# Optimization experiments

Hardware: AMD Instinct MI355X
Metric: run time of the kernel (lower is better)

The kernel has to match this reference:

```python
import jax, jax.numpy as jnp
import numpy as np

WS = 8      # window_size
NH = 8      # n_heads
EPS = 1e-06


def _rel_coords(ws):
    # Swin-style relative position index table, matches torch buffer construction
    c = np.stack(np.meshgrid(np.arange(ws), np.arange(ws), indexing='ij'))  # [2,ws,ws]
    c = c.reshape(2, -1)                      # [2, L]
    rel = c[:, :, None] - c[:, None, :]       # [2, L, L]
    rel = rel.transpose(1, 2, 0) + (ws - 1)   # [L, L, 2]
    rel[:, :, 0] *= 2 * ws - 1
    return jnp.asarray(rel.sum(-1), dtype=jnp.int32)  # [L, L]


def rms_film(x, t, gw, bw):
    # x: [B,C,H,W], t: [B,d_t]; RMS over channel dim, FiLM scale/shift from t
    g = (t @ gw.T)[:, :, None, None]
    b = (t @ bw.T)[:, :, None, None]
    return g * x * jax.lax.rsqrt(jnp.mean(x * x, axis=1, keepdims=True) + EPS) + b


def window_attn(x, wq, wk, wv, wo_w, wo_b, rpb):
    B, C, H, W = x.shape
    h, w = H // WS, W // WS
    L = WS * WS
    dh = C // NH
    # partition into windows: [B, h, w, L, C]
    xw = x.reshape(B, C, h, WS, w, WS).transpose(0, 2, 4, 3, 5, 1).reshape(B, h, w, L, C)

    def heads(p):
        y = xw @ p.T  # Linear, no bias
        return y.reshape(B, h, w, L, NH, dh).transpose(0, 1, 2, 4, 3, 5)  # [B,h,w,n,L,dh]

    q, k, v = heads(wq), heads(wk), heads(wv)
    bias = rpb[:, _rel_coords(WS)]  # [NH, L, L] gather from bias table
    attn = jnp.einsum('bhwnld,bhwnmd->bhwnlm', q, k) / float(np.sqrt(dh)) + bias
    o = jnp.einsum('bhwnlm,bhwnmd->bhwnld', jax.nn.softmax(attn, axis=-1), v)
    # merge windows, channel order (n c): [B, NH*dh, H, W]
    o = o.reshape(B, h, w, NH, WS, WS, dh).transpose(0, 3, 6, 1, 4, 2, 5).reshape(B, C, H, W)
    # 1x1 conv output projection (with bias)
    return jnp.einsum('bchw,oc->bohw', o, wo_w) + wo_b[None, :, None, None]


def convnext(x, t, dw_w, dw_b, gw, bw, w1, b1, w2, b2):
    # 7x7 depthwise conv, pad 3
    y = jax.lax.conv_general_dilated(
        x, dw_w, window_strides=(1, 1), padding=[(3, 3), (3, 3)],
        dimension_numbers=('NCHW', 'OIHW', 'NCHW'), feature_group_count=x.shape[1])
    y = y + dw_b[None, :, None, None]
    y = rms_film(y, t, gw, bw).transpose(0, 2, 3, 1)  # -> NHWC
    y = jax.nn.gelu(y @ w1.T + b1, approximate=False) @ w2.T + b2
    return y.transpose(0, 3, 1, 2)


def setup_inputs() -> dict:
    key = jax.random.key(0)
    ks = jax.random.split(key, 16)
    D, DT, B, H, W = 256, 256, 8, 128, 128
    DH = 4 * D
    n = lambda k, s: jax.random.normal(k, s, jnp.float32) * 0.02
    return dict(
        x=jax.random.normal(ks[0], (B, D, H, W), jnp.float32),
        t=jax.random.normal(ks[1], (B, DT), jnp.float32),
        an_g=n(ks[2], (D, DT)), an_b=n(ks[3], (D, DT)),
        wq=n(ks[4], (D, D)), wk=n(ks[5], (D, D)), wv=n(ks[6], (D, D)),
        wo_w=n(ks[7], (D, D)), wo_b=jnp.zeros((D,), jnp.float32),
        rpb=n(ks[8], (NH, (2 * WS - 1) ** 2)),
        dw_w=n(ks[9], (D, 1, 7, 7)), dw_b=jnp.zeros((D,), jnp.float32),
        fn_g=n(ks[10], (D, DT)), fn_b=n(ks[11], (D, DT)),
        w1=n(ks[12], (DH, D)), b1=jnp.zeros((DH,), jnp.float32),
        w2=n(ks[13], (D, DH)), b2=jnp.zeros((D,), jnp.float32))


def reference(x, t, an_g, an_b, wq, wk, wv, wo_w, wo_b, rpb,
              dw_w, dw_b, fn_g, fn_b, w1, b1, w2, b2):
    x = x + window_attn(rms_film(x, t, an_g, an_b), wq, wk, wv, wo_w, wo_b, rpb)
    return x + convnext(x, t, dw_w, dw_b, fn_g, fn_b, w1, b1, w2, b2)
```

## Files before the change

### kernel.cpp

```cpp
#include <hip/hip_runtime.h>
#include <math.h>

typedef __attribute__((ext_vector_type(8))) short bf16x8_t;
typedef __attribute__((ext_vector_type(4))) float f32x4;

__device__ __forceinline__ unsigned short f2bf(float f) {
  unsigned int u = __builtin_bit_cast(unsigned int, f);
  u += 0x7FFFu + ((u >> 16) & 1u);
  return (unsigned short)(u >> 16);
}
__device__ __forceinline__ float bf2f(unsigned short h) {
  unsigned int u = ((unsigned int)h) << 16;
  return __builtin_bit_cast(float, u);
}

typedef const __attribute__((address_space(1))) void* as1cv;
typedef __attribute__((address_space(3))) void* as3v;

__device__ __forceinline__ void gld_lds16(const unsigned short* g, unsigned short* l) {
  __builtin_amdgcn_global_load_lds((as1cv)g, (as3v)l, 16, 0, 0);
}

__global__ __launch_bounds__(256) void tvec_kernel(const float* __restrict__ t,
    const float* __restrict__ an_g, const float* __restrict__ an_b,
    const float* __restrict__ fn_g, const float* __restrict__ fn_b,
    float* __restrict__ gvec) {
  int d = threadIdx.x;
  int b = blockIdx.x;
  int m = blockIdx.y;
  __shared__ float ts[256];
  ts[d] = t[b * 256 + d];
  __syncthreads();
  const float* W = (m == 0) ? an_g : (m == 1) ? an_b : (m == 2) ? fn_g : fn_b;
  float acc = 0.f;
  #pragma unroll 8
  for (int k = 0; k < 256; ++k) acc += ts[k] * W[d * 256 + k];
  gvec[(m * 8 + b) * 256 + d] = acc;
}

__global__ __launch_bounds__(256) void wconv_kernel(const float* __restrict__ wq,
    const float* __restrict__ wk, const float* __restrict__ wv, const float* __restrict__ wo,
    const float* __restrict__ w1, const float* __restrict__ w2,
    unsigned short* __restrict__ outp) {
  int i = blockIdx.x * 256 + threadIdx.x;
  const float* src; int off;
  if      (i <  65536) { src = wq; off = 0; }
  else if (i < 131072) { src = wk; off = 65536; }
  else if (i < 196608) { src = wv; off = 131072; }
  else if (i < 262144) { src = wo; off = 196608; }
  else if (i < 524288) { src = w1; off = 262144; }
  else                 { src = w2; off = 524288; }
  outp[i] = f2bf(src[i - off]);
}

template<int IS_BF, int WX>
__global__ __launch_bounds__(256) void film_kernel(const void* __restrict__ in_,
    const float* __restrict__ gvec, int gsel, unsigned short* __restrict__ outbf,
    unsigned short* __restrict__ xbf) {
  const float* inf = (const float*)in_;
  const unsigned short* inb = (const unsigned short*)in_;
  int blk = blockIdx.x;
  int b = blk >> 8;
  int p0 = (blk & 255) << 6;
  int lane = threadIdx.x & 63;
  int cg = threadIdx.x >> 6;
  __shared__ unsigned short vals[64][264];
  __shared__ float ssred[4][64];
  __shared__ float rinvs[64];
  size_t base = ((size_t)b << 22) + p0;
  float ss = 0.f;
  #pragma unroll 4
  for (int ci = 0; ci < 64; ++ci) {
    int c = (cg << 6) + ci;
    size_t idx = base + ((size_t)c << 14) + lane;
    float v = IS_BF ? bf2f(inb[idx]) : inf[idx];
    ss += v * v;
    unsigned short hv = f2bf(v);
    vals[lane][c] = hv;
    if (WX) xbf[idx] = hv;
  }
  ssred[cg][lane] = ss;
  __syncthreads();
  if (threadIdx.x < 64) {
    float s = ssred[0][threadIdx.x] + ssred[1][threadIdx.x] + ssred[2][threadIdx.x] + ssred[3][threadIdx.x];
    rinvs[threadIdx.x] = rsqrtf(s * (1.0f / 256.0f) + 1e-6f);
  }
  __syncthreads();
  int pix = threadIdx.x >> 2;
  int c0 = (threadIdx.x & 3) << 6;
  float rv = rinvs[pix];
  const float* gp = gvec + ((gsel * 2 + 0) * 8 + b) * 256;
  const float* bp = gvec + ((gsel * 2 + 1) * 8 + b) * 256;
  unsigned short* orow = outbf + (((size_t)b << 14) + p0 + pix) * 256 + c0;
  #pragma unroll
  for (int ch = 0; ch < 8; ++ch) {
    bf16x8_t pack;
    #pragma unroll
    for (int e = 0; e < 8; ++e) {
      int c = c0 + ch * 8 + e;
      float v = bf2f(vals[pix][c]);
      float o = gp[c] * v * rv + bp[c];
      pack[e] = (short)f2bf(o);
    }
    *(bf16x8_t*)(orow + ch * 8) = pack;
  }
}

template<int DO_GELU>
__global__ __launch_bounds__(256) void gemm_kernel(const unsigned short* __restrict__ A,
    const unsigned short* __restrict__ Bw, const float* __restrict__ bias,
    unsigned short* __restrict__ outp, int K, int N) {
  __shared__ unsigned short As[128 * 64];
  __shared__ unsigned short Bs[128 * 64];
  int tid = threadIdx.x;
  int m0 = blockIdx.x << 7;
  int n0 = blockIdx.y << 7;
  int w = tid >> 6, lane = tid & 63;
  int wm = (w >> 1) << 6, wn = (w & 1) << 6;
  f32x4 acc[4][4];
  #pragma unroll
  for (int mi = 0; mi < 4; ++mi)
    #pragma unroll
    for (int ni = 0; ni < 4; ++ni)
      acc[mi][ni] = (f32x4){0.f, 0.f, 0.f, 0.f};

  for (int k0 = 0; k0 < K; k0 += 64) {
    #pragma unroll
    for (int r2 = 0; r2 < 4; ++r2) {
      int linear = (r2 << 8) + tid;
      int row = linear >> 3;
      int ch = linear & 7;
      gld_lds16(A  + (size_t)(m0 + row) * K + k0 + ch * 8, As + linear * 8);
      gld_lds16(Bw + (size_t)(n0 + row) * K + k0 + ch * 8, Bs + linear * 8);
    }
    __syncthreads();
    #pragma unroll
    for (int kk = 0; kk < 64; kk += 32) {
      bf16x8_t af[4], bq[4];
      int lr = lane & 15;
      int lk = ((lane >> 4) << 3) + kk;
      #pragma unroll
      for (int mi = 0; mi < 4; ++mi)
        af[mi] = *(const bf16x8_t*)(As + ((wm + (mi << 4) + lr) << 6) + lk);
      #pragma unroll
      for (int ni = 0; ni < 4; ++ni)
        bq[ni] = *(const bf16x8_t*)(Bs + ((wn + (ni << 4) + lr) << 6) + lk);
      #pragma unroll
      for (int mi = 0; mi < 4; ++mi)
        #pragma unroll
        for (int ni = 0; ni < 4; ++ni)
          acc[mi][ni] = __builtin_amdgcn_mfma_f32_16x16x32_bf16(af[mi], bq[ni], acc[mi][ni], 0, 0, 0);
    }
    __syncthreads();
  }
  int lr = lane & 15, lg = lane >> 4;
  #pragma unroll
  for (int mi = 0; mi < 4; ++mi) {
    #pragma unroll
    for (int ni = 0; ni < 4; ++ni) {
      int col = n0 + wn + (ni << 4) + lr;
      int row = m0 + wm + (mi << 4) + (lg << 2);
      f32x4 a = acc[mi][ni];
      #pragma unroll
      for (int i = 0; i < 4; ++i) {
        float v = a[i];
        if (DO_GELU) {
          v += bias[col];
          v = 0.5f * v * (1.0f + erff(v * 0.70710678118654752f));
        }
        outp[(size_t)(row + i) * N + col] = f2bf(v);
      }
    }
  }
}

__global__ __launch_bounds__(256) void gemm_qkv_kernel(const unsigned short* __restrict__ A,
    const unsigned short* __restrict__ Bw, unsigned short* __restrict__ outq,
    unsigned short* __restrict__ outk, unsigned short* __restrict__ outvt) {
  __shared__ unsigned short smem[16384];
  unsigned short* As = smem;
  unsigned short* Bs = smem + 8192;
  const int K = 256;
  int tid = threadIdx.x;
  int m0 = blockIdx.x << 7;
  int n0 = blockIdx.y << 7;
  int w = tid >> 6, lane = tid & 63;
  int wm = (w >> 1) << 6, wn = (w & 1) << 6;
  f32x4 acc[4][4];
  #pragma unroll
  for (int mi = 0; mi < 4; ++mi)
    #pragma unroll
    for (int ni = 0; ni < 4; ++ni)
      acc[mi][ni] = (f32x4){0.f, 0.f, 0.f, 0.f};

  for (int k0 = 0; k0 < K; k0 += 64) {
    #pragma unroll
    for (int r2 = 0; r2 < 4; ++r2) {
      int linear = (r2 << 8) + tid;
      int row = linear >> 3;
      int ch = linear & 7;
      gld_lds16(A  + (size_t)(m0 + row) * K + k0 + ch * 8, As + linear * 8);
      gld_lds16(Bw + (size_t)(n0 + row) * K + k0 + ch * 8, Bs + linear * 8);
    }
    __syncthreads();
    #pragma unroll
    for (int kk = 0; kk < 64; kk += 32) {
      bf16x8_t af[4], bq[4];
      int lr = lane & 15;
      int lk = ((lane >> 4) << 3) + kk;
      #pragma unroll
      for (int mi = 0; mi < 4; ++mi)
        af[mi] = *(const bf16x8_t*)(As + ((wm + (mi << 4) + lr) << 6) + lk);
      #pragma unroll
      for (int ni = 0; ni < 4; ++ni)
        bq[ni] = *(const bf16x8_t*)(Bs + ((wn + (ni << 4) + lr) << 6) + lk);
      #pragma unroll
      for (int mi = 0; mi < 4; ++mi)
        #pragma unroll
        for (int ni = 0; ni < 4; ++ni)
          acc[mi][ni] = __builtin_amdgcn_mfma_f32_16x16x32_bf16(af[mi], bq[ni], acc[mi][ni], 0, 0, 0);
    }
    __syncthreads();
  }

  int lr = lane & 15, lg = lane >> 4;
  if (n0 < 512) {
    unsigned short* dst = (n0 < 256) ? outq : outk;
    #pragma unroll
    for (int mi = 0; mi < 4; ++mi) {
      #pragma unroll
      for (int ni = 0; ni < 4; ++ni) {
        int col = (n0 & 255) + wn + (ni << 4) + lr;
        int row = m0 + wm + (mi << 4) + (lg << 2);
        f32x4 a = acc[mi][ni];
        #pragma unroll
        for (int i = 0; i < 4; ++i)
          dst[(size_t)(row + i) * 256 + col] = f2bf(a[i]);
      }
    }
  } else {
    #pragma unroll
    for (int mi = 0; mi < 4; ++mi)
      #pragma unroll
      for (int ni = 0; ni < 4; ++ni) {
        int cl = wn + (ni << 4) + lr;
        int rl = wm + (mi << 4) + (lg << 2);
        f32x4 a = acc[mi][ni];
        #pragma unroll
        for (int i = 0; i < 4; ++i)
          smem[cl * 128 + rl + i] = f2bf(a[i]);
      }
    __syncthreads();
    int cl = tid >> 1;
    int half = tid & 1;
    int b = m0 >> 14;
    int pix = (m0 & 16383) + half * 64;
    int c = (n0 - 512) + cl;
    const unsigned short* srow = smem + cl * 128 + half * 64;
    unsigned short* orow = outvt + ((size_t)b * 256 + c) * 16384 + pix;
    #pragma unroll
    for (int jj = 0; jj < 8; ++jj)
      *(bf16x8_t*)(orow + jj * 8) = *(const bf16x8_t*)(srow + jj * 8);
  }
}

__global__ __launch_bounds__(256) void gemm_wof_kernel(const unsigned short* __restrict__ A,
    const unsigned short* __restrict__ Bw, const float* __restrict__ bias,
    const unsigned short* __restrict__ xbf, unsigned short* __restrict__ outp) {
  __shared__ unsigned short smem[16384];
  unsigned short* As = smem;
  unsigned short* Bs = smem + 8192;
  const int K = 256;
  int tid = threadIdx.x;
  int m0 = blockIdx.x << 7;
  int n0 = blockIdx.y << 7;
  int w = tid >> 6, lane = tid & 63;
  int wm = (w >> 1) << 6, wn = (w & 1) << 6;
  f32x4 acc[4][4];
  #pragma unroll
  for (int mi = 0; mi < 4; ++mi)
    #pragma unroll
    for (int ni = 0; ni < 4; ++ni)
      acc[mi][ni] = (f32x4){0.f, 0.f, 0.f, 0.f};

  for (int k0 = 0; k0 < K; k0 += 64) {
    #pragma unroll
    for (int r2 = 0; r2 < 4; ++r2) {
      int linear = (r2 << 8) + tid;
      int row = linear >> 3;
      int ch = linear & 7;
      gld_lds16(A  + (size_t)(m0 + row) * K + k0 + ch * 8, As + linear * 8);
      gld_lds16(Bw + (size_t)(n0 + row) * K + k0 + ch * 8, Bs + linear * 8);
    }
    __syncthreads();
    #pragma unroll
    for (int kk = 0; kk < 64; kk += 32) {
      bf16x8_t af[4], bq[4];
      int lr = lane & 15;
      int lk = ((lane >> 4) << 3) + kk;
      #pragma unroll
      for (int mi = 0; mi < 4; ++mi)
        af[mi] = *(const bf16x8_t*)(As + ((wm + (mi << 4) + lr) << 6) + lk);
      #pragma unroll
      for (int ni = 0; ni < 4; ++ni)
        bq[ni] = *(const bf16x8_t*)(Bs + ((wn + (ni << 4) + lr) << 6) + lk);
      #pragma unroll
      for (int mi = 0; mi < 4; ++mi)
        #pragma unroll
        for (int ni = 0; ni < 4; ++ni)
          acc[mi][ni] = __builtin_amdgcn_mfma_f32_16x16x32_bf16(af[mi], bq[ni], acc[mi][ni], 0, 0, 0);
    }
    __syncthreads();
  }

  int lr = lane & 15, lg = lane >> 4;
  #pragma unroll
  for (int mi = 0; mi < 4; ++mi)
    #pragma unroll
    for (int ni = 0; ni < 4; ++ni) {
      int cl = wn + (ni << 4) + lr;
      int rl = wm + (mi << 4) + (lg << 2);
      f32x4 a = acc[mi][ni];
      #pragma unroll
      for (int i = 0; i < 4; ++i)
        smem[cl * 128 + rl + i] = f2bf(a[i]);
    }
  __syncthreads();

  int cl = tid >> 1;
  int half = tid & 1;
  int b = m0 >> 14;
  int pix = (m0 & 16383) + half * 64;
  int c = n0 + cl;
  const unsigned short* srow = smem + cl * 128 + half * 64;
  size_t gbase = ((size_t)b * 256 + c) * 16384 + pix;
  const unsigned short* xrow = xbf + gbase;
  unsigned short* orow = outp + gbase;
  float bb = bias[c];
  #pragma unroll
  for (int jj = 0; jj < 8; ++jj) {
    bf16x8_t sv = *(const bf16x8_t*)(srow + jj * 8);
    bf16x8_t xv = *(const bf16x8_t*)(xrow + jj * 8);
    bf16x8_t ov;
    #pragma unroll
    for (int e = 0; e < 8; ++e)
      ov[e] = (short)f2bf(bf2f((unsigned short)sv[e]) + bf2f((unsigned short)xv[e]) + bb);
    *(bf16x8_t*)(orow + jj * 8) = ov;
  }
}

__global__ __launch_bounds__(256) void gemm2f_kernel(const unsigned short* __restrict__ A,
    const unsigned short* __restrict__ Bw, const float* __restrict__ bias,
    const unsigned short* __restrict__ x1, float* __restrict__ outp, int m_base) {
  __shared__ unsigned short smem[16384];
  unsigned short* As = smem;
  unsigned short* Bs = smem + 8192;
  const int K = 1024, N = 256;
  int tid = threadIdx.x;
  int m0 = blockIdx.x << 7;
  int n0 = blockIdx.y << 7;
  int w = tid >> 6, lane = tid & 63;
  int wm = (w >> 1) << 6, wn = (w & 1) << 6;
  f32x4 acc[4][4];
  #pragma unroll
  for (int mi = 0; mi < 4; ++mi)
    #pragma unroll
    for (int ni = 0; ni < 4; ++ni)
      acc[mi][ni] = (f32x4){0.f, 0.f, 0.f, 0.f};

  for (int k0 = 0; k0 < K; k0 += 64) {
    #pragma unroll
    for (int r2 = 0; r2 < 4; ++r2) {
      int linear = (r2 << 8) + tid;
      int row = linear >> 3;
      int ch = linear & 7;
      gld_lds16(A  + (size_t)(m0 + row) * K + k0 + ch * 8, As + linear * 8);
      gld_lds16(Bw + (size_t)(n0 + row) * K + k0 + ch * 8, Bs + linear * 8);
    }
    __syncthreads();
    #pragma unroll
    for (int kk = 0; kk < 64; kk += 32) {
      bf16x8_t af[4], bq[4];
      int lr = lane & 15;
      int lk = ((lane >> 4) << 3) + kk;
      #pragma unroll
      for (int mi = 0; mi < 4; ++mi)
        af[mi] = *(const bf16x8_t*)(As + ((wm + (mi << 4) + lr) << 6) + lk);
      #pragma unroll
      for (int ni = 0; ni < 4; ++ni)
        bq[ni] = *(const bf16x8_t*)(Bs + ((wn + (ni << 4) + lr) << 6) + lk);
      #pragma unroll
      for (int mi = 0; mi < 4; ++mi)
        #pragma unroll
        for (int ni = 0; ni < 4; ++ni)
          acc[mi][ni] = __builtin_amdgcn_mfma_f32_16x16x32_bf16(af[mi], bq[ni], acc[mi][ni], 0, 0, 0);
    }
    __syncthreads();
  }

  int lr = lane & 15, lg = lane >> 4;
  #pragma unroll
  for (int mi = 0; mi < 4; ++mi)
    #pragma unroll
    for (int ni = 0; ni < 4; ++ni) {
      int cl = wn + (ni << 4) + lr;
      int rl = wm + (mi << 4) + (lg << 2);
      f32x4 a = acc[mi][ni];
      #pragma unroll
      for (int i = 0; i < 4; ++i)
        smem[cl * 128 + rl + i] = f2bf(a[i]);
    }
  __syncthreads();

  int cl = tid >> 1;
  int half = tid & 1;
  int pglob0 = m_base + m0;
  int b = pglob0 >> 14;
  int pix = (pglob0 & 16383) + half * 64;
  int c = n0 + cl;
  const unsigned short* srow = smem + cl * 128 + half * 64;
  size_t gbase = ((size_t)b * 256 + c) * 16384 + pix;
  const unsigned short* xrow = x1 + gbase;
  float* orow = outp + gbase;
  float bb = bias[c];
  #pragma unroll
  for (int jj = 0; jj < 8; ++jj) {
    bf16x8_t sv = *(const bf16x8_t*)(srow + jj * 8);
    bf16x8_t xv = *(const bf16x8_t*)(xrow + jj * 8);
    #pragma unroll
    for (int e = 0; e < 8; ++e)
      orow[jj * 8 + e] = bf2f((unsigned short)sv[e]) + bf2f((unsigned short)xv[e]) + bb;
  }
}

__global__ __launch_bounds__(256, 4) void attn_kernel(const unsigned short* __restrict__ qg,
    const unsigned short* __restrict__ kg, const unsigned short* __restrict__ vt,
    const float* __restrict__ rpb, unsigned short* __restrict__ og) {
  __shared__ float rpbf[1800];
  __shared__ unsigned short pbuf[4][16 * 72];
  int wi = (blockIdx.x & 7) * 256 + (blockIdx.x >> 3);
  int b = wi >> 8, wh = (wi >> 4) & 15, ww = wi & 15;
  int tid = threadIdx.x;
  int w = tid >> 6, lane = tid & 63;
  int g = lane >> 4, lr = lane & 15;
  for (int idx = tid; idx < 1800; idx += 256) rpbf[idx] = rpb[idx];
  __syncthreads();

  int rowpix = (wh * 8) * 128 + ww * 8;
  size_t ibase = ((size_t)b << 14) + rowpix;
  unsigned short* pb = pbuf[w];
  const float scale = 0.17677669529663689f;

  #pragma unroll 1
  for (int hh = 0; hh < 2; ++hh) {
    int h = w * 2 + hh;
    bf16x8_t qf[4], kf[4];
    #pragma unroll
    for (int t = 0; t < 4; ++t) {
      size_t tok = ibase + (size_t)(t * 2 + (lr >> 3)) * 128 + (lr & 7);
      qf[t] = *(const bf16x8_t*)(qg + tok * 256 + h * 32 + g * 8);
      kf[t] = *(const bf16x8_t*)(kg + tok * 256 + h * 32 + g * 8);
    }
    bf16x8_t vfr[2][2];
    #pragma unroll
    for (int ks = 0; ks < 2; ++ks)
      #pragma unroll
      for (int dt = 0; dt < 2; ++dt) {
        size_t plane = (size_t)b * 256 + h * 32 + dt * 16 + lr;
        vfr[ks][dt] = *(const bf16x8_t*)(vt + (plane << 14) + rowpix + (size_t)(ks * 4 + g) * 128);
      }
    const float* rb = &rpbf[h * 225];

    #pragma unroll 1
    for (int qt = 0; qt < 4; ++qt) {
      f32x4 sacc[4];
      #pragma unroll
      for (int kt = 0; kt < 4; ++kt)
        sacc[kt] = __builtin_amdgcn_mfma_f32_16x16x32_bf16(qf[qt], kf[kt],
                     (f32x4){0.f, 0.f, 0.f, 0.f}, 0, 0, 0);
      float sums[4];
      #pragma unroll
      for (int i = 0; i < 4; ++i) {
        int q = qt * 16 + g * 4 + i;
        int il = q >> 3, jl = q & 7;
        float v[4];
        #pragma unroll
        for (int kt = 0; kt < 4; ++kt) {
          int kv = kt * 16 + lr;
          v[kt] = sacc[kt][i] * scale + rb[(il - (kv >> 3) + 7) * 15 + (jl - (kv & 7) + 7)];
        }
        float mx = fmaxf(fmaxf(v[0], v[1]), fmaxf(v[2], v[3]));
        mx = fmaxf(mx, __shfl_xor(mx, 1));
        mx = fmaxf(mx, __shfl_xor(mx, 2));
        mx = fmaxf(mx, __shfl_xor(mx, 4));
        mx = fmaxf(mx, __shfl_xor(mx, 8));
        float sm = 0.f;
        #pragma unroll
        for (int kt = 0; kt < 4; ++kt) { v[kt] = __expf(v[kt] - mx); sm += v[kt]; }
        sm += __shfl_xor(sm, 1);
        sm += __shfl_xor(sm, 2);
        sm += __shfl_xor(sm, 4);
        sm += __shfl_xor(sm, 8);
        sums[i] = sm;
        #pragma unroll
        for (int kt = 0; kt < 4; ++kt)
          pb[(g * 4 + i) * 72 + kt * 16 + lr] = f2bf(v[kt]);
      }
      f32x4 oacc[2] = {(f32x4){0.f, 0.f, 0.f, 0.f}, (f32x4){0.f, 0.f, 0.f, 0.f}};
      #pragma unroll
      for (int ks = 0; ks < 2; ++ks) {
        bf16x8_t pf = *(const bf16x8_t*)(pb + lr * 72 + ks * 32 + g * 8);
        oacc[0] = __builtin_amdgcn_mfma_f32_16x16x32_bf16(pf, vfr[ks][0], oacc[0], 0, 0, 0);
        oacc[1] = __builtin_amdgcn_mfma_f32_16x16x32_bf16(pf, vfr[ks][1], oacc[1], 0, 0, 0);
      }
      #pragma unroll
      for (int i = 0; i < 4; ++i) {
        int q = qt * 16 + g * 4 + i;
        float inv = 1.0f / sums[i];
        size_t tok = ibase + (size_t)(q >> 3) * 128 + (q & 7);
        unsigned int packed0 = f2bf(oacc[0][i] * inv);
        unsigned int packed1 = f2bf(oacc[1][i] * inv);
        og[tok * 256 + h * 32 + lr] = (unsigned short)packed0;
        og[tok * 256 + h * 32 + 16 + lr] = (unsigned short)packed1;
      }
    }
  }
}

__global__ __launch_bounds__(256) void dwconv_kernel(const unsigned short* __restrict__ x1,
    const float* __restrict__ w, const float* __restrict__ bias, unsigned short* __restrict__ outp) {
  int bc = blockIdx.y;
  int c = bc & 255;
  int y0 = blockIdx.x << 6;
  __shared__ unsigned short tile[70 * 144];
  __shared__ float wf[49];
  const unsigned short* plane = x1 + ((size_t)bc << 14);
  int tid = threadIdx.x;

  for (int idx = tid; idx < 70 * 16; idx += 256) {
    int row = idx >> 4, ch = idx & 15;
    int gy = y0 - 3 + row;
    bf16x8_t v = (bf16x8_t){0, 0, 0, 0, 0, 0, 0, 0};
    if (gy >= 0 && gy < 128) v = *(const bf16x8_t*)(plane + gy * 128 + ch * 8);
    *(bf16x8_t*)(&tile[row * 144 + 8 + ch * 8]) = v;
  }
  for (int idx = tid; idx < 70 * 6; idx += 256) {
    int row = idx / 6, e = idx % 6;
    int col = (e < 3) ? (5 + e) : (133 + e);
    tile[row * 144 + col] = 0;
  }
  if (tid < 49) wf[tid] = w[c * 49 + tid];
  __syncthreads();

  int r = tid >> 2;
  int c0 = (tid & 3) << 5;
  float acc[32];
  float bb = bias[c];
  #pragma unroll
  for (int i = 0; i < 32; ++i) acc[i] = bb;

  #pragma unroll
  for (int u = 0; u < 7; ++u) {
    const unsigned short* rowp = &tile[(r + u) * 144 + c0];
    float f[48];
    #pragma unroll
    for (int k = 0; k < 6; ++k) {
      bf16x8_t v = *(const bf16x8_t*)(rowp + k * 8);
      #pragma unroll
      for (int e = 0; e < 8; ++e) f[k * 8 + e] = bf2f((unsigned short)v[e]);
    }
    #pragma unroll
    for (int t = 0; t < 7; ++t) {
      float wv = wf[u * 7 + t];
      #pragma unroll
      for (int i = 0; i < 32; ++i) acc[i] += f[i + 5 + t] * wv;
    }
  }

  unsigned short* orow = outp + ((size_t)bc << 14) + (size_t)(y0 + r) * 128 + c0;
  #pragma unroll
  for (int k = 0; k < 4; ++k) {
    bf16x8_t v;
    #pragma unroll
    for (int e = 0; e < 8; ++e) v[e] = (short)f2bf(acc[k * 8 + e]);
    *(bf16x8_t*)(orow + k * 8) = v;
  }
}

extern "C" void kernel_launch(void* const* d_in, const int* in_sizes, int n_in,
                              void* d_out, int out_size, void* d_ws, size_t ws_size,
                              hipStream_t stream) {
  const float* x    = (const float*)d_in[0];
  const float* t    = (const float*)d_in[1];
  const float* an_g = (const float*)d_in[2];
  const float* an_b = (const float*)d_in[3];
  const float* wq   = (const float*)d_in[4];
  const float* wk   = (const float*)d_in[5];
  const float* wv   = (const float*)d_in[6];
  const float* wo_w = (const float*)d_in[7];
  const float* wo_b = (const float*)d_in[8];
  const float* rpb  = (const float*)d_in[9];
  const float* dw_w = (const float*)d_in[10];
  const float* dw_b = (const float*)d_in[11];
  const float* fn_g = (const float*)d_in[12];
  const float* fn_b = (const float*)d_in[13];
  const float* w1   = (const float*)d_in[14];
  const float* b1   = (const float*)d_in[15];
  const float* w2   = (const float*)d_in[16];
  const float* b2   = (const float*)d_in[17];
  float* outp = (float*)d_out;

  char* ws = (char*)d_ws;
  const size_t MB = 1024ull * 1024ull;
  float* gvec = (float*)ws;
  unsigned short* wbf = (unsigned short*)(ws + 32768);
  unsigned short* P = (unsigned short*)(ws + 2 * MB);
  unsigned short* Q = (unsigned short*)(ws + 66 * MB);
  unsigned short* R = (unsigned short*)(ws + 130 * MB);
  unsigned short* xbf  = (unsigned short*)d_out;
  unsigned short* vbuf = (unsigned short*)((char*)d_out + 64 * MB);

  unsigned short* wo_bf = wbf + 196608;
  unsigned short* w1_bf = wbf + 262144;
  unsigned short* w2_bf = wbf + 524288;

  tvec_kernel<<<dim3(8, 4), 256, 0, stream>>>(t, an_g, an_b, fn_g, fn_b, gvec);
  wconv_kernel<<<3072, 256, 0, stream>>>(wq, wk, wv, wo_w, w1, w2, wbf);

  film_kernel<0, 1><<<2048, 256, 0, stream>>>(x, gvec, 0, P, xbf);

  gemm_qkv_kernel<<<dim3(1024, 6), 256, 0, stream>>>(P, wbf, Q, R, vbuf);

  attn_kernel<<<2048, 256, 0, stream>>>(Q, R, vbuf, rpb, P);

  gemm_wof_kernel<<<dim3(1024, 2), 256, 0, stream>>>(P, wo_bf, wo_b, xbf, R);

  dwconv_kernel<<<dim3(2, 2048), 256, 0, stream>>>(R, dw_w, dw_b, Q);
  film_kernel<1, 0><<<2048, 256, 0, stream>>>(Q, gvec, 1, P, nullptr);

  for (int qtr = 0; qtr < 4; ++qtr) {
    int m_base = qtr * 32768;
    gemm_kernel<1><<<dim3(256, 8), 256, 0, stream>>>(P + (size_t)m_base * 256, w1_bf, b1, Q, 256, 1024);
    gemm2f_kernel<<<dim3(256, 2), 256, 0, stream>>>(Q, w2_bf, b2, R, outp, m_base);
  }
}
```

Measured before the change: 984.9 us.

## Fuse MLP GEMM1+GELU+GEMM2 into one kernel and split QKV GEMM

Replaces the four-chunk pair of MLP GEMMs with a single kernel per 64-row tile. Each block keeps the z tile in LDS with an XOR swizzle and loops over 128-wide hidden slices, computing GELU into a small LDS buffer before accumulating the second GEMM in registers. This removes the 1024-wide hidden activation round trip through global memory. Weight fragments are now loaded directly from global/L2 without LDS staging, which may cost bandwidth. The fused QKV launch is also split into three separate GEMM launches.

New measurement: 891.9 us. 1.1x faster.

```diff
diff --git a/kernel.cpp b/kernel.cpp
--- a/kernel.cpp
+++ b/kernel.cpp
@@ -174,9 +174,8 @@
   }
 }
 
-__global__ __launch_bounds__(256) void gemm_qkv_kernel(const unsigned short* __restrict__ A,
-    const unsigned short* __restrict__ Bw, unsigned short* __restrict__ outq,
-    unsigned short* __restrict__ outk, unsigned short* __restrict__ outvt) {
+__global__ __launch_bounds__(256) void gemm_t_kernel(const unsigned short* __restrict__ A,
+    const unsigned short* __restrict__ Bw, unsigned short* __restrict__ outp) {
   __shared__ unsigned short smem[16384];
   unsigned short* As = smem;
   unsigned short* Bs = smem + 8192;
@@ -224,44 +223,29 @@
   }
 
   int lr = lane & 15, lg = lane >> 4;
-  if (n0 < 512) {
-    unsigned short* dst = (n0 < 256) ? outq : outk;
-    #pragma unroll
-    for (int mi = 0; mi < 4; ++mi) {
-      #pragma unroll
-      for (int ni = 0; ni < 4; ++ni) {
-        int col = (n0 & 255) + wn + (ni << 4) + lr;
-        int row = m0 + wm + (mi << 4) + (lg << 2);
-        f32x4 a = acc[mi][ni];
-        #pragma unroll
-        for (int i = 0; i < 4; ++i)
-          dst[(size_t)(row + i) * 256 + col] = f2bf(a[i]);
-      }
-    }
-  } else {
-    #pragma unroll
-    for (int mi = 0; mi < 4; ++mi)
-      #pragma unroll
-      for (int ni = 0; ni < 4; ++ni) {
-        int cl = wn + (ni << 4) + lr;
-        int rl = wm + (mi << 4) + (lg << 2);
-        f32x4 a = acc[mi][ni];
-        #pragma unroll
-        for (int i = 0; i < 4; ++i)
-          smem[cl * 128 + rl + i] = f2bf(a[i]);
-      }
-    __syncthreads();
-    int cl = tid >> 1;
-    int half = tid & 1;
-    int b = m0 >> 14;
-    int pix = (m0 & 16383) + half * 64;
-    int c = (n0 - 512) + cl;
-    const unsigned short* srow = smem + cl * 128 + half * 64;
-    unsigned short* orow = outvt + ((size_t)b * 256 + c) * 16384 + pix;
-    #pragma unroll
-    for (int jj = 0; jj < 8; ++jj)
-      *(bf16x8_t*)(orow + jj * 8) = *(const bf16x8_t*)(srow + jj * 8);
-  }
+  #pragma unroll
+  for (int mi = 0; mi < 4; ++mi)
+    #pragma unroll
+    for (int ni = 0; ni < 4; ++ni) {
+      int cl = wn + (ni << 4) + lr;
+      int rl = wm + (mi << 4) + (lg << 2);
+      f32x4 a = acc[mi][ni];
+      #pragma unroll
+      for (int i = 0; i < 4; ++i)
+        smem[cl * 128 + rl + i] = f2bf(a[i]);
+    }
+  __syncthreads();
+
+  int cl = tid >> 1;
+  int half = tid & 1;
+  int b = m0 >> 14;
+  int pix = (m0 & 16383) + half * 64;
+  int c = n0 + cl;
+  const unsigned short* srow = smem + cl * 128 + half * 64;
+  unsigned short* orow = outp + ((size_t)b * 256 + c) * 16384 + pix;
+  #pragma unroll
+  for (int jj = 0; jj < 8; ++jj)
+    *(bf16x8_t*)(orow + jj * 8) = *(const bf16x8_t*)(srow + jj * 8);
 }
 
 __global__ __launch_bounds__(256) void gemm_wof_kernel(const unsigned short* __restrict__ A,
@@ -349,18 +333,26 @@
   }
 }
 
-__global__ __launch_bounds__(256) void gemm2f_kernel(const unsigned short* __restrict__ A,
-    const unsigned short* __restrict__ Bw, const float* __restrict__ bias,
-    const unsigned short* __restrict__ x1, float* __restrict__ outp, int m_base) {
-  __shared__ unsigned short smem[16384];
-  unsigned short* As = smem;
-  unsigned short* Bs = smem + 8192;
-  const int K = 1024, N = 256;
+__global__ __launch_bounds__(256, 3) void gemm_mlp_kernel(const unsigned short* __restrict__ z,
+    const unsigned short* __restrict__ w1, const float* __restrict__ b1,
+    const unsigned short* __restrict__ w2, const float* __restrict__ b2,
+    const unsigned short* __restrict__ x1, float* __restrict__ outp) {
+  __shared__ unsigned short ztile[64 * 256];
+  __shared__ unsigned short hbuf[64 * 136];
   int tid = threadIdx.x;
-  int m0 = blockIdx.x << 7;
-  int n0 = blockIdx.y << 7;
+  int m0 = blockIdx.x << 6;
   int w = tid >> 6, lane = tid & 63;
-  int wm = (w >> 1) << 6, wn = (w & 1) << 6;
+  int g = lane >> 4, lr = lane & 15;
+
+  #pragma unroll
+  for (int r2 = 0; r2 < 8; ++r2) {
+    int linear = (r2 << 8) + tid;
+    int row = linear >> 5;
+    int ch = linear & 31;
+    gld_lds16(z + (size_t)(m0 + row) * 256 + ((ch ^ (row & 7)) << 3), ztile + linear * 8);
+  }
+  __syncthreads();
+
   f32x4 acc[4][4];
   #pragma unroll
   for (int mi = 0; mi < 4; ++mi)
@@ -368,64 +360,90 @@
     for (int ni = 0; ni < 4; ++ni)
       acc[mi][ni] = (f32x4){0.f, 0.f, 0.f, 0.f};
 
-  for (int k0 = 0; k0 < K; k0 += 64) {
-    #pragma unroll
-    for (int r2 = 0; r2 < 4; ++r2) {
-      int linear = (r2 << 8) + tid;
-      int row = linear >> 3;
-      int ch = linear & 7;
-      gld_lds16(A  + (size_t)(m0 + row) * K + k0 + ch * 8, As + linear * 8);
-      gld_lds16(Bw + (size_t)(n0 + row) * K + k0 + ch * 8, Bs + linear * 8);
-    }
-    __syncthreads();
-    #pragma unroll
-    for (int kk = 0; kk < 64; kk += 32) {
-      bf16x8_t af[4], bq[4];
-      int lr = lane & 15;
-      int lk = ((lane >> 4) << 3) + kk;
-      #pragma unroll
-      for (int mi = 0; mi < 4; ++mi)
-        af[mi] = *(const bf16x8_t*)(As + ((wm + (mi << 4) + lr) << 6) + lk);
+  #pragma unroll 1
+  for (int j = 0; j < 8; ++j) {
+    f32x4 hacc[4][2];
+    #pragma unroll
+    for (int mi = 0; mi < 4; ++mi) {
+      hacc[mi][0] = (f32x4){0.f, 0.f, 0.f, 0.f};
+      hacc[mi][1] = (f32x4){0.f, 0.f, 0.f, 0.f};
+    }
+    #pragma unroll
+    for (int k32 = 0; k32 < 8; ++k32) {
+      bf16x8_t af[4], bq[2];
+      int cidx = (k32 << 2) + g;
+      #pragma unroll
+      for (int mi = 0; mi < 4; ++mi) {
+        int row = mi * 16 + lr;
+        af[mi] = *(const bf16x8_t*)(ztile + row * 256 + ((cidx ^ (row & 7)) << 3));
+      }
+      int kb = (k32 << 5) + (g << 3);
+      #pragma unroll
+      for (int ni = 0; ni < 2; ++ni)
+        bq[ni] = *(const bf16x8_t*)(w1 + (size_t)(j * 128 + w * 32 + ni * 16 + lr) * 256 + kb);
+      #pragma unroll
+      for (int mi = 0; mi < 4; ++mi)
+        #pragma unroll
+        for (int ni = 0; ni < 2; ++ni)
+          hacc[mi][ni] = __builtin_amdgcn_mfma_f32_16x16x32_bf16(af[mi], bq[ni], hacc[mi][ni], 0, 0, 0);
+    }
+    #pragma unroll
+    for (int ni = 0; ni < 2; ++ni) {
+      int hcol = w * 32 + ni * 16 + lr;
+      float bb = b1[j * 128 + hcol];
+      #pragma unroll
+      for (int mi = 0; mi < 4; ++mi) {
+        #pragma unroll
+        for (int i = 0; i < 4; ++i) {
+          float v = hacc[mi][ni][i] + bb;
+          v = 0.5f * v * (1.0f + erff(v * 0.70710678118654752f));
+          hbuf[(mi * 16 + g * 4 + i) * 136 + hcol] = f2bf(v);
+        }
+      }
+    }
+    __syncthreads();
+    #pragma unroll
+    for (int ks = 0; ks < 4; ++ks) {
+      int kb = (ks << 5) + (g << 3);
+      bf16x8_t pf[4], bq2[4];
+      #pragma unroll
+      for (int mi = 0; mi < 4; ++mi)
+        pf[mi] = *(const bf16x8_t*)(hbuf + (mi * 16 + lr) * 136 + kb);
       #pragma unroll
       for (int ni = 0; ni < 4; ++ni)
-        bq[ni] = *(const bf16x8_t*)(Bs + ((wn + (ni << 4) + lr) << 6) + lk);
+        bq2[ni] = *(const bf16x8_t*)(w2 + (size_t)(w * 64 + ni * 16 + lr) * 1024 + j * 128 + kb);
       #pragma unroll
       for (int mi = 0; mi < 4; ++mi)
         #pragma unroll
         for (int ni = 0; ni < 4; ++ni)
-          acc[mi][ni] = __builtin_amdgcn_mfma_f32_16x16x32_bf16(af[mi], bq[ni], acc[mi][ni], 0, 0, 0);
-    }
-    __syncthreads();
-  }
-
-  int lr = lane & 15, lg = lane >> 4;
+          acc[mi][ni] = __builtin_amdgcn_mfma_f32_16x16x32_bf16(pf[mi], bq2[ni], acc[mi][ni], 0, 0, 0);
+    }
+    __syncthreads();
+  }
+
+  unsigned short* stg = ztile;
   #pragma unroll
   for (int mi = 0; mi < 4; ++mi)
     #pragma unroll
     for (int ni = 0; ni < 4; ++ni) {
-      int cl = wn + (ni << 4) + lr;
-      int rl = wm + (mi << 4) + (lg << 2);
+      int cl = w * 64 + ni * 16 + lr;
+      int rl = mi * 16 + g * 4;
       f32x4 a = acc[mi][ni];
       #pragma unroll
       for (int i = 0; i < 4; ++i)
-        smem[cl * 128 + rl + i] = f2bf(a[i]);
-    }
-  __syncthreads();
-
-  int cl = tid >> 1;
-  int half = tid & 1;
-  int pglob0 = m_base + m0;
-  int b = pglob0 >> 14;
-  int pix = (pglob0 & 16383) + half * 64;
-  int c = n0 + cl;
-  const unsigned short* srow = smem + cl * 128 + half * 64;
+        stg[cl * 64 + ((rl + i) ^ ((cl & 7) << 3))] = f2bf(a[i]);
+    }
+  __syncthreads();
+  int c = tid;
+  int b = m0 >> 14;
+  int pix = m0 & 16383;
   size_t gbase = ((size_t)b * 256 + c) * 16384 + pix;
   const unsigned short* xrow = x1 + gbase;
   float* orow = outp + gbase;
-  float bb = bias[c];
+  float bb = b2[c];
   #pragma unroll
   for (int jj = 0; jj < 8; ++jj) {
-    bf16x8_t sv = *(const bf16x8_t*)(srow + jj * 8);
+    bf16x8_t sv = *(const bf16x8_t*)(stg + c * 64 + ((jj ^ (c & 7)) << 3));
     bf16x8_t xv = *(const bf16x8_t*)(xrow + jj * 8);
     #pragma unroll
     for (int e = 0; e < 8; ++e)
@@ -518,10 +536,8 @@
         int q = qt * 16 + g * 4 + i;
         float inv = 1.0f / sums[i];
         size_t tok = ibase + (size_t)(q >> 3) * 128 + (q & 7);
-        unsigned int packed0 = f2bf(oacc[0][i] * inv);
-        unsigned int packed1 = f2bf(oacc[1][i] * inv);
-        og[tok * 256 + h * 32 + lr] = (unsigned short)packed0;
-        og[tok * 256 + h * 32 + 16 + lr] = (unsigned short)packed1;
+        og[tok * 256 + h * 32 + lr] = f2bf(oacc[0][i] * inv);
+        og[tok * 256 + h * 32 + 16 + lr] = f2bf(oacc[1][i] * inv);
       }
     }
   }
@@ -620,6 +636,9 @@
   unsigned short* xbf  = (unsigned short*)d_out;
   unsigned short* vbuf = (unsigned short*)((char*)d_out + 64 * MB);
 
+  unsigned short* wq_bf = wbf;
+  unsigned short* wk_bf = wbf + 65536;
+  unsigned short* wv_bf = wbf + 131072;
   unsigned short* wo_bf = wbf + 196608;
   unsigned short* w1_bf = wbf + 262144;
   unsigned short* w2_bf = wbf + 524288;
@@ -629,7 +648,9 @@
 
   film_kernel<0, 1><<<2048, 256, 0, stream>>>(x, gvec, 0, P, xbf);
 
-  gemm_qkv_kernel<<<dim3(1024, 6), 256, 0, stream>>>(P, wbf, Q, R, vbuf);
+  gemm_kernel<0><<<dim3(1024, 2), 256, 0, stream>>>(P, wq_bf, nullptr, Q, 256, 256);
+  gemm_kernel<0><<<dim3(1024, 2), 256, 0, stream>>>(P, wk_bf, nullptr, R, 256, 256);
+  gemm_t_kernel<<<dim3(1024, 2), 256, 0, stream>>>(P, wv_bf, vbuf);
 
   attn_kernel<<<2048, 256, 0, stream>>>(Q, R, vbuf, rpb, P);
 
@@ -638,9 +659,5 @@
   dwconv_kernel<<<dim3(2, 2048), 256, 0, stream>>>(R, dw_w, dw_b, Q);
   film_kernel<1, 0><<<2048, 256, 0, stream>>>(Q, gvec, 1, P, nullptr);
 
-  for (int qtr = 0; qtr < 4; ++qtr) {
-    int m_base = qtr * 32768;
-    gemm_kernel<1><<<dim3(256, 8), 256, 0, stream>>>(P + (size_t)m_base * 256, w1_bf, b1, Q, 256, 1024);
-    gemm2f_kernel<<<dim3(256, 2), 256, 0, stream>>>(Q, w2_bf, b2, R, outp, m_base);
-  }
-}
+  gemm_mlp_kernel<<<2048, 256, 0, stream>>>(P, w1_bf, b1, w2_bf, b2, R, outp);
+}
```
